# Kernel tuning notes

Measured on AMD Instinct MI355X. Metric: run time of the kernel, lower is better.

## Reference

```python
import jax, jax.numpy as jnp
import numpy as np
from jax import lax

B, T, I, H = 64, 512, 512, 1024


def setup_inputs() -> dict:
    key = jax.random.key(0)
    k1, k2, k3, k4 = jax.random.split(key, 4)
    # Gates stacked in order: resetgate, updategate, hidden_update (matches forward()).
    inp = jax.random.normal(k1, (B, T, I), dtype=jnp.float32)
    W_in_stacked = jax.random.normal(k2, (I, 3 * H), dtype=jnp.float32) * 0.1
    W_hid_stacked = jax.random.normal(k3, (H, 3 * H), dtype=jnp.float32) * 0.1
    b_stacked = jax.random.normal(k4, (3 * H,), dtype=jnp.float32) * 0.1
    hid_init = jnp.zeros((1, H), dtype=jnp.float32)
    return {"inp": inp, "W_in_stacked": W_in_stacked,
            "W_hid_stacked": W_hid_stacked, "b_stacked": b_stacked,
            "hid_init": hid_init}


def reference(inp, W_in_stacked, W_hid_stacked, b_stacked, hid_init):
    n_units = hid_init.shape[1]
    n_batch = inp.shape[0]
    # Precompute the input contribution for all timesteps (as the original does
    # with one big mm before the loop): [B,T,3H] -> [T,B,3H] seq-first.
    x = jnp.einsum('bti,ig->btg', inp, W_in_stacked) + b_stacked
    x = jnp.swapaxes(x, 0, 1)
    h0 = jnp.broadcast_to(hid_init, (n_batch, n_units))

    def step(h_prev, x_t):
        hid_input = h_prev @ W_hid_stacked  # [B, 3H]
        r = jax.nn.sigmoid(x_t[:, :n_units] + hid_input[:, :n_units])
        u = jax.nn.sigmoid(x_t[:, n_units:2 * n_units]
                           + hid_input[:, n_units:2 * n_units])
        c = jnp.tanh(x_t[:, 2 * n_units:] + r * hid_input[:, 2 * n_units:])
        h_new = (1.0 - u) * h_prev + u * c
        return h_new, None

    h_final, _ = lax.scan(step, h0, x)
    return h_final  # [B, n_units]
```

## Files before the change

kernel.cpp:

```cpp
#include <hip/hip_runtime.h>
#include <hip/hip_fp16.h>
#include <math.h>

typedef _Float16 h16;
typedef __attribute__((ext_vector_type(4))) _Float16 h16x4;
typedef __attribute__((ext_vector_type(8))) _Float16 h16x8;
typedef __attribute__((ext_vector_type(4))) float f32x4;
typedef unsigned long long u64;

#define T_SEQ 512
#define NB    64
#define NI    512
#define NH    1024
#define N3H   3072

__device__ __forceinline__ u64 cload64(const u64* p) {
  return __hip_atomic_load(p, __ATOMIC_RELAXED, __HIP_MEMORY_SCOPE_AGENT);
}
__device__ __forceinline__ void cstore64(u64* p, u64 v) {
  __hip_atomic_store(p, v, __ATOMIC_RELAXED, __HIP_MEMORY_SCOPE_AGENT);
}
__device__ __forceinline__ unsigned cload32(const unsigned* p) {
  return __hip_atomic_load(p, __ATOMIC_RELAXED, __HIP_MEMORY_SCOPE_AGENT);
}
__device__ __forceinline__ void cstore32(unsigned* p, unsigned v) {
  __hip_atomic_store(p, v, __ATOMIC_RELAXED, __HIP_MEMORY_SCOPE_AGENT);
}

union H4 { u64 q; h16x4 v; };
union F8 { u64 q[2]; h16x8 v; };


__global__ void gru_init_h(const float* __restrict__ hid0,
                           u64* __restrict__ hfrag) {
  int W = blockIdx.x * blockDim.x + threadIdx.x;
  if (W >= 16384) return;
  int bg = W >> 12;
  int w  = W & 4095;
  int kt = w >> 7;
  int lp = (w >> 1) & 63;
  int q  = w & 1;
  int cb = kt * 32 + ((lp >> 4) & 3) * 8 + q * 4;
  H4 o;
  #pragma unroll
  for (int j = 0; j < 4; ++j) o.v[j] = (h16)hid0[cb + j];
  hfrag[(size_t)bg * 4096 + w] = o.q;
}

#define P1_BM 128
#define P1_BK 32

__device__ __forceinline__ int p1swz(int r, int k) {
  return r * P1_BK + ((((k >> 3) ^ (r & 3)) << 3) | (k & 7));
}

__global__ __launch_bounds__(256, 2) void gru_xgemm(
    const float* __restrict__ inp, const float* __restrict__ Win,
    const float* __restrict__ bstk, h16* __restrict__ x) {
  __shared__ h16 sAh[2][P1_BM * P1_BK];
  __shared__ h16 sAl[2][P1_BM * P1_BK];
  __shared__ h16 sBh[2][P1_BM * P1_BK];
  __shared__ h16 sBl[2][P1_BM * P1_BK];

  const int tid = threadIdx.x;
  const int l = tid & 63;
  const int w = tid >> 6;
  const int wm = (w >> 1) * 64, wn = (w & 1) * 64;
  const int mi = blockIdx.x, ni = blockIdx.y;

  const int sr  = tid >> 1;
  const int skh = (tid & 1) * 16;

  const float* aSrcBase = inp + (size_t)(sr & 63) * (T_SEQ * NI)
                              + (size_t)(mi * 2 + (sr >> 6)) * NI + skh;
  const float* bSrcBase = Win + (size_t)skh * N3H + ni * 128 + sr;

  f32x4 acc[4][4] = {};
  float aReg[16];
  float bReg[16];

  auto stage_load = [&](int ks) {
    const float* ap = aSrcBase + ks * P1_BK;
    #pragma unroll
    for (int jg = 0; jg < 4; ++jg) {
      f32x4 v = *(const f32x4*)(ap + jg * 4);
      aReg[jg*4+0] = v[0]; aReg[jg*4+1] = v[1];
      aReg[jg*4+2] = v[2]; aReg[jg*4+3] = v[3];
    }
    const float* bp = bSrcBase + (size_t)ks * P1_BK * N3H;
    #pragma unroll
    for (int j = 0; j < 16; ++j) bReg[j] = bp[(size_t)j * N3H];
  };

  auto stage_write = [&](int buf) {
    #pragma unroll
    for (int jg = 0; jg < 4; ++jg) {
      int idx = p1swz(sr, skh + jg * 4);
      h16x4 hi, lo;
      #pragma unroll
      for (int j = 0; j < 4; ++j) {
        float v = aReg[jg*4+j];
        h16 h = (h16)v; hi[j] = h; lo[j] = (h16)(v - (float)h);
      }
      *(h16x4*)&sAh[buf][idx] = hi;
      *(h16x4*)&sAl[buf][idx] = lo;
      #pragma unroll
      for (int j = 0; j < 4; ++j) {
        float v = bReg[jg*4+j];
        h16 h = (h16)v; hi[j] = h; lo[j] = (h16)(v - (float)h);
      }
      *(h16x4*)&sBh[buf][idx] = hi;
      *(h16x4*)&sBl[buf][idx] = lo;
    }
  };

  auto compute = [&](int buf) {
    const int k0 = (l >> 4) * 8;
    h16x8 bh[4], bl[4];
    #pragma unroll
    for (int nt = 0; nt < 4; ++nt) {
      int idx = p1swz(wn + nt * 16 + (l & 15), k0);
      bh[nt] = *(const h16x8*)&sBh[buf][idx];
      bl[nt] = *(const h16x8*)&sBl[buf][idx];
    }
    #pragma unroll
    for (int mt = 0; mt < 4; ++mt) {
      int idx = p1swz(wm + mt * 16 + (l & 15), k0);
      h16x8 ah = *(const h16x8*)&sAh[buf][idx];
      h16x8 al = *(const h16x8*)&sAl[buf][idx];
      #pragma unroll
      for (int nt = 0; nt < 4; ++nt) {
        acc[mt][nt] = __builtin_amdgcn_mfma_f32_16x16x32_f16(ah, bh[nt], acc[mt][nt], 0, 0, 0);
        acc[mt][nt] = __builtin_amdgcn_mfma_f32_16x16x32_f16(ah, bl[nt], acc[mt][nt], 0, 0, 0);
        acc[mt][nt] = __builtin_amdgcn_mfma_f32_16x16x32_f16(al, bh[nt], acc[mt][nt], 0, 0, 0);
      }
    }
  };

  stage_load(0);
  stage_write(0);
  __syncthreads();
  for (int ks = 0; ks < 16; ++ks) {
    int buf = ks & 1;
    if (ks < 15) stage_load(ks + 1);
    compute(buf);
    if (ks < 15) stage_write(buf ^ 1);
    __syncthreads();
  }

  const int t = mi * 2 + (wm >> 6);
  const int rrb = (l >> 4) * 4;
  #pragma unroll
  for (int nt = 0; nt < 4; ++nt) {
    int colhi = ni * 8 + (wn >> 4) + nt;
    int gg  = colhi >> 6;
    int cgx = colhi & 63;
    float bias = bstk[(colhi << 4) + (l & 15)];
    #pragma unroll
    for (int mt = 0; mt < 4; ++mt) {
      h16x4 v;
      #pragma unroll
      for (int i = 0; i < 4; ++i) v[i] = (h16)(acc[mt][nt][i] + bias);
      size_t idx = ((((size_t)t * 3 + gg) * 64 + cgx) * 4 + mt) * 256
                 + (size_t)(l & 15) * 16 + rrb;
      *(h16x4*)&x[idx] = v;
    }
  }
}

__global__ __launch_bounds__(192, 1) void gru_steps(
    const float* __restrict__ Whid,
    const h16* __restrict__ x,
    u64* __restrict__ hfrag,
    unsigned* __restrict__ tags,
    const float* __restrict__ hid0,
    float* __restrict__ out) {
  __shared__ h16 U[3 * 32 * 64 * 8];
  __shared__ h16 tq[16 * 20];

  const int tid = threadIdx.x;
  const int l = tid & 63;
  const int g = tid >> 6;
  const int cg = blockIdx.x & 63;
  const int bg = blockIdx.x >> 6;

  {
    const float* base = Whid + (size_t)g * NH + (size_t)cg * 16 + (l & 15);
    for (int kt = 0; kt < 32; ++kt) {
      const float* src = base + (size_t)(kt * 32 + (l >> 4) * 8) * N3H;
      h16x8 v;
      #pragma unroll
      for (int j = 0; j < 8; ++j) v[j] = (h16)src[(size_t)j * N3H];
      *(h16x8*)&U[(size_t)((g * 32 + kt) * 64 + l) * 8] = v;
    }
  }
  __syncthreads();
  if (g != 0) return;

  const int rr0 = (l >> 4) * 4, cc = l & 15;

  float hq[4];
  {
    float h0 = hid0[cg * 16 + cc];
    #pragma unroll
    for (int i = 0; i < 4; ++i) hq[i] = h0;
  }

  const char* xb0 = (const char*)(x + ((((size_t)0 * 64 + cg) * 4 + bg) * 256)
                                    + (size_t)cc * 16 + rr0);
  const char* xb1 = xb0 + 64 * 4 * 256 * 2;
  const char* xb2 = xb1 + 64 * 4 * 256 * 2;
  u64 xq0 = *(const u64*)xb0, xq1 = *(const u64*)xb1, xq2 = *(const u64*)xb2;

  const int dstw = cg * 64 + ((l >> 4) >> 1) * 32 + (l & 15) * 2 + ((l >> 4) & 1);

  for (int s = 1; s <= T_SEQ; ++s) {
    const int par = (s - 1) & 1;
    const u64* plane = hfrag + ((size_t)par * 4 + bg) * 4096;
    const unsigned* tgin = tags + (par * 4 + bg) * 64;

    {
      const unsigned need = (unsigned)(s - 1);
      int spincnt = 0;
      for (;;) {
        unsigned tv = cload32(tgin + l);
        if (__all((int)(tv >= need))) break;
        __builtin_amdgcn_s_sleep(1);
        if (++spincnt > 200000) break;
      }
    }
    __builtin_amdgcn_sched_barrier(0);

    u64 xn0 = xq0, xn1 = xq1, xn2 = xq2;
    if (s < T_SEQ) {
      xn0 = *(const u64*)(xb0 + (size_t)s * 393216);
      xn1 = *(const u64*)(xb1 + (size_t)s * 393216);
      xn2 = *(const u64*)(xb2 + (size_t)s * 393216);
    }

    u64 A[64];
    #pragma unroll
    for (int kt = 0; kt < 32; ++kt) {
      A[2 * kt]     = cload64(plane + ((size_t)kt * 64 + l) * 2);
      A[2 * kt + 1] = cload64(plane + ((size_t)kt * 64 + l) * 2 + 1);
    }

    f32x4 ac0 = {}, ac1 = {}, ac2 = {};
    #pragma unroll
    for (int kt = 0; kt < 32; ++kt) {
      F8 f; f.q[0] = A[2 * kt]; f.q[1] = A[2 * kt + 1];
      h16x8 b0 = *(const h16x8*)&U[(size_t)((0 * 32 + kt) * 64 + l) * 8];
      h16x8 b1 = *(const h16x8*)&U[(size_t)((1 * 32 + kt) * 64 + l) * 8];
      h16x8 b2 = *(const h16x8*)&U[(size_t)((2 * 32 + kt) * 64 + l) * 8];
      ac0 = __builtin_amdgcn_mfma_f32_16x16x32_f16(f.v, b0, ac0, 0, 0, 0);
      ac1 = __builtin_amdgcn_mfma_f32_16x16x32_f16(f.v, b1, ac1, 0, 0, 0);
      ac2 = __builtin_amdgcn_mfma_f32_16x16x32_f16(f.v, b2, ac2, 0, 0, 0);
    }

    H4 xr; xr.q = xq0;
    H4 xu; xu.q = xq1;
    H4 xc; xc.q = xq2;
    #pragma unroll
    for (int i = 0; i < 4; ++i) {
      float r = 1.0f / (1.0f + __expf(-((float)xr.v[i] + ac0[i])));
      float u = 1.0f / (1.0f + __expf(-((float)xu.v[i] + ac1[i])));
      float z = (float)xc.v[i] + r * ac2[i];
      float e = __expf(2.0f * z);
      float c = 1.0f - 2.0f / (e + 1.0f);
      float hn = (1.0f - u) * hq[i] + u * c;
      hq[i] = hn;
      tq[(rr0 + i) * 20 + cc] = (h16)hn;
      if (s == T_SEQ) out[(size_t)(bg * 16 + rr0 + i) * NH + cg * 16 + cc] = hn;
    }

    H4 pv; pv.v = *(const h16x4*)&tq[(l & 15) * 20 + (l >> 4) * 4];
    u64* outp = hfrag + ((size_t)(s & 1) * 4 + bg) * 4096;
    cstore64(outp + dstw, pv.q);
    asm volatile("s_waitcnt vmcnt(0)" ::: "memory");
    __builtin_amdgcn_sched_barrier(0);
    if (l == 0)
      cstore32(tags + ((s & 1) * 4 + bg) * 64 + cg, (unsigned)s);

    xq0 = xn0; xq1 = xn1; xq2 = xn2;
  }
}

extern "C" void kernel_launch(void* const* d_in, const int* in_sizes, int n_in,
                              void* d_out, int out_size, void* d_ws, size_t ws_size,
                              hipStream_t stream) {
  const float* inp  = (const float*)d_in[0];
  const float* Win  = (const float*)d_in[1];
  const float* Whid = (const float*)d_in[2];
  const float* bstk = (const float*)d_in[3];
  const float* hid0 = (const float*)d_in[4];
  float* out = (float*)d_out;

  char* ws = (char*)d_ws;
  const size_t xBytes = (size_t)T_SEQ * NB * N3H * sizeof(h16);
  const size_t hBytes = (size_t)2 * 4 * 4096 * sizeof(u64);
  const size_t tBytes = 2 * 4 * 64 * sizeof(unsigned);
  if (ws_size < xBytes + hBytes + tBytes) return;

  h16* x = (h16*)ws;
  u64* hfrag = (u64*)(ws + xBytes);
  unsigned* tags = (unsigned*)(ws + xBytes + hBytes);

  hipMemsetAsync(tags, 0, tBytes, stream);

  gru_init_h<<<dim3(16384 / 256), dim3(256), 0, stream>>>(hid0, hfrag);

  dim3 g1(32768 / P1_BM, N3H / 128);
  gru_xgemm<<<g1, dim3(256), 0, stream>>>(inp, Win, bstk, x);

  gru_steps<<<dim3(256), dim3(192), 0, stream>>>(Whid, x, hfrag, tags, hid0, out);
}
```

Before: 2.548 ms.

## Embed step tags in fp16 hidden-state mantissa bits, drop separate flag sync

```diff
diff --git a/kernel.cpp b/kernel.cpp
--- a/kernel.cpp
+++ b/kernel.cpp
@@ -14,21 +14,22 @@
 #define NH    1024
 #define N3H   3072
 
+#define TAGM 0x0001000100010001ULL
+
 __device__ __forceinline__ u64 cload64(const u64* p) {
   return __hip_atomic_load(p, __ATOMIC_RELAXED, __HIP_MEMORY_SCOPE_AGENT);
 }
 __device__ __forceinline__ void cstore64(u64* p, u64 v) {
   __hip_atomic_store(p, v, __ATOMIC_RELAXED, __HIP_MEMORY_SCOPE_AGENT);
 }
-__device__ __forceinline__ unsigned cload32(const unsigned* p) {
-  return __hip_atomic_load(p, __ATOMIC_RELAXED, __HIP_MEMORY_SCOPE_AGENT);
-}
-__device__ __forceinline__ void cstore32(unsigned* p, unsigned v) {
-  __hip_atomic_store(p, v, __ATOMIC_RELAXED, __HIP_MEMORY_SCOPE_AGENT);
-}
 
 union H4 { u64 q; h16x4 v; };
 union F8 { u64 q[2]; h16x8 v; };
+
+__device__ __forceinline__ u64 tagpat(unsigned e) {
+  return (u64)(e & 1) | ((u64)((e >> 1) & 1) << 16)
+       | ((u64)((e >> 2) & 1) << 32) | ((u64)((e >> 3) & 1) << 48);
+}
 
 
 __global__ void gru_init_h(const float* __restrict__ hid0,
@@ -40,11 +41,11 @@
   int kt = w >> 7;
   int lp = (w >> 1) & 63;
   int q  = w & 1;
-  int cb = kt * 32 + ((lp >> 4) & 3) * 8 + q * 4;
+  int cb = kt * 32 + (lp >> 4) * 8 + q * 4;
   H4 o;
   #pragma unroll
   for (int j = 0; j < 4; ++j) o.v[j] = (h16)hid0[cb + j];
-  hfrag[(size_t)bg * 4096 + w] = o.q;
+  hfrag[(size_t)bg * 4096 + w] = o.q & ~TAGM;
 }
 
 #define P1_BM 128
@@ -172,7 +173,6 @@
     const float* __restrict__ Whid,
     const h16* __restrict__ x,
     u64* __restrict__ hfrag,
-    unsigned* __restrict__ tags,
     const float* __restrict__ hid0,
     float* __restrict__ out) {
   __shared__ h16 U[3 * 32 * 64 * 8];
@@ -215,21 +215,8 @@
   const int dstw = cg * 64 + ((l >> 4) >> 1) * 32 + (l & 15) * 2 + ((l >> 4) & 1);
 
   for (int s = 1; s <= T_SEQ; ++s) {
-    const int par = (s - 1) & 1;
-    const u64* plane = hfrag + ((size_t)par * 4 + bg) * 4096;
-    const unsigned* tgin = tags + (par * 4 + bg) * 64;
-
-    {
-      const unsigned need = (unsigned)(s - 1);
-      int spincnt = 0;
-      for (;;) {
-        unsigned tv = cload32(tgin + l);
-        if (__all((int)(tv >= need))) break;
-        __builtin_amdgcn_s_sleep(1);
-        if (++spincnt > 200000) break;
-      }
-    }
-    __builtin_amdgcn_sched_barrier(0);
+    const u64* plane = hfrag + ((size_t)((s - 1) & 1) * 4 + bg) * 4096;
+    const u64 patc = tagpat((((unsigned)(s - 1)) >> 1) & 15u);
 
     u64 xn0 = xq0, xn1 = xq1, xn2 = xq2;
     if (s < T_SEQ) {
@@ -238,24 +225,58 @@
       xn2 = *(const u64*)(xb2 + (size_t)s * 393216);
     }
 
-    u64 A[64];
-    #pragma unroll
-    for (int kt = 0; kt < 32; ++kt) {
-      A[2 * kt]     = cload64(plane + ((size_t)kt * 64 + l) * 2);
-      A[2 * kt + 1] = cload64(plane + ((size_t)kt * 64 + l) * 2 + 1);
-    }
-
     f32x4 ac0 = {}, ac1 = {}, ac2 = {};
-    #pragma unroll
-    for (int kt = 0; kt < 32; ++kt) {
-      F8 f; f.q[0] = A[2 * kt]; f.q[1] = A[2 * kt + 1];
-      h16x8 b0 = *(const h16x8*)&U[(size_t)((0 * 32 + kt) * 64 + l) * 8];
-      h16x8 b1 = *(const h16x8*)&U[(size_t)((1 * 32 + kt) * 64 + l) * 8];
-      h16x8 b2 = *(const h16x8*)&U[(size_t)((2 * 32 + kt) * 64 + l) * 8];
-      ac0 = __builtin_amdgcn_mfma_f32_16x16x32_f16(f.v, b0, ac0, 0, 0, 0);
-      ac1 = __builtin_amdgcn_mfma_f32_16x16x32_f16(f.v, b1, ac1, 0, 0, 0);
-      ac2 = __builtin_amdgcn_mfma_f32_16x16x32_f16(f.v, b2, ac2, 0, 0, 0);
-    }
+    u64 w0[16], w1[16], w2[16], w3[16];
+
+    auto loadc = [&](u64 (&W)[16], int c) {
+      #pragma unroll
+      for (int j = 0; j < 16; ++j) {
+        int kt = c * 8 + (j >> 1);
+        W[j] = cload64(plane + ((size_t)kt * 64 + l) * 2 + (j & 1));
+      }
+    };
+    auto fixc = [&](u64 (&W)[16], int c) {
+      for (int tries = 0; tries < 30000; ++tries) {
+        unsigned bad = 0;
+        #pragma unroll
+        for (int j = 0; j < 16; ++j)
+          bad |= (((W[j] ^ patc) & TAGM) != 0ULL) ? (1u << j) : 0u;
+        if (bad == 0) break;
+        if (tries > 4) __builtin_amdgcn_s_sleep(1);
+        #pragma unroll
+        for (int j = 0; j < 16; ++j) {
+          int kt = c * 8 + (j >> 1);
+          if (bad & (1u << j))
+            W[j] = cload64(plane + ((size_t)kt * 64 + l) * 2 + (j & 1));
+        }
+      }
+    };
+    auto mfmac = [&](u64 (&W)[16], int c) {
+      #pragma unroll
+      for (int j = 0; j < 8; ++j) {
+        int kt = c * 8 + j;
+        F8 f; f.q[0] = W[2 * j]; f.q[1] = W[2 * j + 1];
+        h16x8 b0 = *(const h16x8*)&U[(size_t)((0 * 32 + kt) * 64 + l) * 8];
+        h16x8 b1 = *(const h16x8*)&U[(size_t)((1 * 32 + kt) * 64 + l) * 8];
+        h16x8 b2 = *(const h16x8*)&U[(size_t)((2 * 32 + kt) * 64 + l) * 8];
+        ac0 = __builtin_amdgcn_mfma_f32_16x16x32_f16(f.v, b0, ac0, 0, 0, 0);
+        ac1 = __builtin_amdgcn_mfma_f32_16x16x32_f16(f.v, b1, ac1, 0, 0, 0);
+        ac2 = __builtin_amdgcn_mfma_f32_16x16x32_f16(f.v, b2, ac2, 0, 0, 0);
+      }
+    };
+
+    loadc(w0, 0);
+    loadc(w1, 1);
+    fixc(w0, 0);
+    loadc(w2, 2);
+    mfmac(w0, 0);
+    fixc(w1, 1);
+    loadc(w3, 3);
+    mfmac(w1, 1);
+    fixc(w2, 2);
+    mfmac(w2, 2);
+    fixc(w3, 3);
+    mfmac(w3, 3);
 
     H4 xr; xr.q = xq0;
     H4 xu; xu.q = xq1;
@@ -274,12 +295,9 @@
     }
 
     H4 pv; pv.v = *(const h16x4*)&tq[(l & 15) * 20 + (l >> 4) * 4];
+    u64 word = (pv.q & ~TAGM) | tagpat(((unsigned)s >> 1) & 15u);
     u64* outp = hfrag + ((size_t)(s & 1) * 4 + bg) * 4096;
-    cstore64(outp + dstw, pv.q);
-    asm volatile("s_waitcnt vmcnt(0)" ::: "memory");
-    __builtin_amdgcn_sched_barrier(0);
-    if (l == 0)
-      cstore32(tags + ((s & 1) * 4 + bg) * 64 + cg, (unsigned)s);
+    cstore64(outp + dstw, word);
 
     xq0 = xn0; xq1 = xn1; xq2 = xn2;
   }
@@ -298,19 +316,15 @@
   char* ws = (char*)d_ws;
   const size_t xBytes = (size_t)T_SEQ * NB * N3H * sizeof(h16);
   const size_t hBytes = (size_t)2 * 4 * 4096 * sizeof(u64);
-  const size_t tBytes = 2 * 4 * 64 * sizeof(unsigned);
-  if (ws_size < xBytes + hBytes + tBytes) return;
+  if (ws_size < xBytes + hBytes) return;
 
   h16* x = (h16*)ws;
   u64* hfrag = (u64*)(ws + xBytes);
-  unsigned* tags = (unsigned*)(ws + xBytes + hBytes);
-
-  hipMemsetAsync(tags, 0, tBytes, stream);
 
   gru_init_h<<<dim3(16384 / 256), dim3(256), 0, stream>>>(hid0, hfrag);
 
   dim3 g1(32768 / P1_BM, N3H / 128);
   gru_xgemm<<<g1, dim3(256), 0, stream>>>(inp, Win, bstk, x);
 
-  gru_steps<<<dim3(256), dim3(192), 0, stream>>>(Whid, x, hfrag, tags, hid0, out);
-}
+  gru_steps<<<dim3(256), dim3(192), 0, stream>>>(Whid, x, hfrag, hid0, out);
+}
```

Result: slower. 2.663 ms (+4.5%).
